# Kernel tuning notes

Measured on AMD Instinct MI355X. Metric: run time of the kernel, lower is better.

The kernel has to match this reference:

```python
import jax, jax.numpy as jnp
import numpy as np

N = 100000
E = 3200000
F_IN = 256
HID = 16
N_CLS = 32


def setup_inputs() -> dict:
    key = jax.random.key(0)
    ks = jax.random.split(key, 9)
    x = jax.random.normal(ks[0], (N, F_IN), dtype=jnp.float32)
    edge_index = jax.random.randint(ks[1], (2, E), 0, N, dtype=jnp.int32)
    def glorot(k, fan_in, fan_out):
        s = jnp.sqrt(6.0 / (fan_in + fan_out)).astype(jnp.float32)
        return jax.random.uniform(k, (fan_in, fan_out), jnp.float32, -s, s)
    return {
        "x": x,
        "edge_index": edge_index,
        "W1": glorot(ks[2], F_IN, HID), "b1": jnp.zeros((HID,), jnp.float32),
        "W2": glorot(ks[3], HID, HID), "b2": jnp.zeros((HID,), jnp.float32),
        "W3": glorot(ks[4], HID, N_CLS), "b3": jnp.zeros((N_CLS,), jnp.float32),
    }


def _gcn_conv(h, W, b, src, dst, deg_inv_sqrt):
    # h: [N, d_in] -> [N, d_out]. PyG GCNConv: linear, then D^-1/2 (A+I) D^-1/2 aggregation, then bias.
    h = h @ W                                        # [N, d_out]
    norm = deg_inv_sqrt[src] * deg_inv_sqrt[dst]     # [E]
    msg = h[src] * norm[:, None]                     # [E, d_out]
    agg = jax.ops.segment_sum(msg, dst, num_segments=N)
    # self-loop contribution: norm_ii = deg_inv_sqrt[i]^2
    agg = agg + (deg_inv_sqrt ** 2)[:, None] * h
    return agg + b


def reference(x, edge_index, W1, b1, W2, b2, W3, b3):
    src, dst = edge_index[0], edge_index[1]
    # degree with self-loops (edge weights = 1), computed on dst per PyG gcn_norm
    deg = jax.ops.segment_sum(jnp.ones((E,), jnp.float32), dst, num_segments=N) + 1.0
    deg_inv_sqrt = jax.lax.rsqrt(deg)
    h = jax.nn.elu(_gcn_conv(x, W1, b1, src, dst, deg_inv_sqrt))
    h = jax.nn.elu(_gcn_conv(h, W2, b2, src, dst, deg_inv_sqrt))
    h = jax.nn.elu(_gcn_conv(h, W3, b3, src, dst, deg_inv_sqrt))
    # dropout is identity in eval mode (training=False)
    return jax.nn.log_softmax(h, axis=1)
```

## Files before the change

### kernel.cpp

```cpp
#include <hip/hip_runtime.h>
#include <math.h>

static constexpr int N_NODES = 100000;
static constexpr int N_EDGES = 3200000;
static constexpr int F_INC   = 256;
static constexpr int HIDC    = 16;
static constexpr int NCLS    = 32;

static constexpr int BNODES  = 256;
static constexpr int NBKT    = (N_NODES + BNODES - 1) / BNODES;
static constexpr int CAP     = 9216;
static constexpr int CHUNK   = 4096;
static constexpr int NCHUNK  = (N_EDGES + CHUNK - 1) / CHUNK;
static constexpr int NTILES  = N_NODES / 16;

typedef __attribute__((ext_vector_type(8))) short bf16x8;
typedef __attribute__((ext_vector_type(4))) float f32x4;

__device__ __forceinline__ unsigned pack_bf2(float a, float b) {
    unsigned ua = __float_as_uint(a);
    unsigned ub = __float_as_uint(b);
    ua = (ua + 0x7FFFu + ((ua >> 16) & 1u)) >> 16;
    ub = (ub + 0x7FFFu + ((ub >> 16) & 1u)) & 0xFFFF0000u;
    return ua | ub;
}
__device__ __forceinline__ float bflo(unsigned v) { return __uint_as_float(v << 16); }
__device__ __forceinline__ float bfhi(unsigned v) { return __uint_as_float(v & 0xFFFF0000u); }
__device__ __forceinline__ float elu1(float t) { return t > 0.f ? t : expm1f(t); }

__global__ void k_zero_cur(int* gcur) {
    int i = threadIdx.x;
    if (i < NBKT) gcur[i] = 0;
}

__global__ __launch_bounds__(256) void k_bucket(const int* __restrict__ src,
                                                const int* __restrict__ dst,
                                                int* gcur, unsigned int* __restrict__ slab) {
    __shared__ int hist[512];
    __shared__ int sc[512];
    __shared__ int place[512];
    __shared__ int gbase[512];
    __shared__ unsigned int staging[CHUNK];
    __shared__ unsigned short bid[CHUNK];
    int tid = threadIdx.x;
    int e0 = blockIdx.x * CHUNK;
    int n = min(CHUNK, N_EDGES - e0);
    hist[tid] = 0; hist[tid + 256] = 0;
    __syncthreads();
    unsigned int pay[16];
    int bk[16];
    #pragma unroll
    for (int r = 0; r < 16; ++r) {
        int i = r * 256 + tid;
        bk[r] = -1;
        if (i < n) {
            int e = e0 + i;
            int s = src[e];
            int t = dst[e];
            int b = t >> 8;
            pay[r] = (unsigned)s | ((unsigned)(t & 255) << 24);
            bk[r] = b;
            atomicAdd(&hist[b], 1);
        }
    }
    __syncthreads();
    sc[tid] = hist[tid]; sc[tid + 256] = hist[tid + 256];
    __syncthreads();
    for (int off = 1; off < 512; off <<= 1) {
        int i0 = tid, i1 = tid + 256;
        int v0 = (i0 >= off) ? sc[i0 - off] : 0;
        int v1 = (i1 >= off) ? sc[i1 - off] : 0;
        __syncthreads();
        sc[i0] += v0; sc[i1] += v1;
        __syncthreads();
    }
    {
        int b0 = tid, b1 = tid + 256;
        int o0 = sc[b0] - hist[b0];
        int o1 = sc[b1] - hist[b1];
        place[b0] = o0; place[b1] = o1;
        sc[b0] = o0; sc[b1] = o1;
        if (b0 < NBKT && hist[b0]) gbase[b0] = atomicAdd(&gcur[b0], hist[b0]);
        if (b1 < NBKT && hist[b1]) gbase[b1] = atomicAdd(&gcur[b1], hist[b1]);
    }
    __syncthreads();
    #pragma unroll
    for (int r = 0; r < 16; ++r) {
        if (bk[r] >= 0) {
            int p = atomicAdd(&place[bk[r]], 1);
            staging[p] = pay[r];
            bid[p] = (unsigned short)bk[r];
        }
    }
    __syncthreads();
    for (int i = tid; i < n; i += 256) {
        int b = bid[i];
        int gp = gbase[b] + (i - sc[b]);
        if (gp < CAP) slab[(size_t)b * CAP + gp] = staging[i];
    }
}

__global__ __launch_bounds__(512) void k_csr(const int* __restrict__ gcur,
                                             unsigned int* __restrict__ slab,
                                             int* __restrict__ rowptr,
                                             int* __restrict__ cnt,
                                             float* __restrict__ dis) {
    __shared__ int hist[BNODES];
    __shared__ int lofs[BNODES];
    __shared__ int place[BNODES];
    __shared__ unsigned int reord[CAP];
    int tid = threadIdx.x, b = blockIdx.x;
    if (tid < BNODES) hist[tid] = 0;
    __syncthreads();
    int count = min(gcur[b], CAP);
    unsigned int* sl = slab + (size_t)b * CAP;
    for (int i = tid; i < count; i += 512) atomicAdd(&hist[sl[i] >> 24], 1);
    __syncthreads();
    if (tid < BNODES) lofs[tid] = hist[tid];
    __syncthreads();
    for (int off = 1; off < BNODES; off <<= 1) {
        int v = 0;
        if (tid < BNODES && tid >= off) v = lofs[tid - off];
        __syncthreads();
        if (tid < BNODES) lofs[tid] += v;
        __syncthreads();
    }
    if (tid < BNODES) {
        int ex = lofs[tid] - hist[tid];
        lofs[tid] = ex;
        place[tid] = ex;
        int node = b * BNODES + tid;
        if (node < N_NODES) {
            rowptr[node] = b * CAP + ex;
            cnt[node] = hist[tid];
            dis[node] = rsqrtf((float)hist[tid] + 1.0f);
        }
    }
    __syncthreads();
    for (int i = tid; i < count; i += 512) {
        unsigned int v = sl[i];
        int dl = v >> 24;
        int p = atomicAdd(&place[dl], 1);
        reord[p] = v & 0xFFFFFFu;
    }
    __syncthreads();
    for (int i = tid; i < count; i += 512) sl[i] = reord[i];
}

__global__ __launch_bounds__(256) void k_linear1(const float* __restrict__ x,
                                                 const float* __restrict__ W1,
                                                 const float* __restrict__ dis,
                                                 unsigned* __restrict__ hb) {
    __shared__ float dtile[4][16][18];
    int tid = threadIdx.x;
    int lane = tid & 63;
    int w = tid >> 6;
    int tile = blockIdx.x * 4 + w;
    if (tile >= NTILES) return;
    int g = lane >> 4;
    int r = lane & 15;
    union { uint4 u; bf16x8 v; } bfr[8];
    #pragma unroll
    for (int m = 0; m < 8; ++m) {
        unsigned uu[4];
        #pragma unroll
        for (int t = 0; t < 4; ++t) {
            int k0 = 32 * m + 8 * g + 2 * t;
            uu[t] = pack_bf2(W1[k0 * HIDC + r], W1[(k0 + 1) * HIDC + r]);
        }
        bfr[m].u = make_uint4(uu[0], uu[1], uu[2], uu[3]);
    }
    const float* xrow = x + (size_t)(tile * 16 + r) * F_INC;
    f32x4 acc = {0.f, 0.f, 0.f, 0.f};
    #pragma unroll
    for (int m = 0; m < 8; ++m) {
        int ks = 32 * m + 8 * g;
        float4 va = *(const float4*)(xrow + ks);
        float4 vb = *(const float4*)(xrow + ks + 4);
        union { uint4 u; bf16x8 v; } af;
        af.u = make_uint4(pack_bf2(va.x, va.y), pack_bf2(va.z, va.w),
                          pack_bf2(vb.x, vb.y), pack_bf2(vb.z, vb.w));
        acc = __builtin_amdgcn_mfma_f32_16x16x32_bf16(af.v, bfr[m].v, acc, 0, 0, 0);
    }
    #pragma unroll
    for (int t = 0; t < 4; ++t) dtile[w][4 * g + t][r] = acc[t];
    __builtin_amdgcn_s_waitcnt(0);
    int q = lane & 7;
    #pragma unroll
    for (int h = 0; h < 2; ++h) {
        int rr = (lane >> 3) + 8 * h;
        int node = tile * 16 + rr;
        float dn = dis[node];
        hb[(size_t)node * 8 + q] =
            pack_bf2(dn * dtile[w][rr][2 * q], dn * dtile[w][rr][2 * q + 1]);
    }
}

__device__ __forceinline__ void gather_core(int base, int deg, int q,
                                            const unsigned* __restrict__ csr,
                                            const unsigned* __restrict__ hb,
                                            unsigned sv, float& acc0, float& acc1) {
    acc0 = bflo(sv); acc1 = bfhi(sv);
    int j = 0;
    for (; j + 3 < deg; j += 4) {
        int s0 = csr[base + j];
        int s1 = csr[base + j + 1];
        int s2 = csr[base + j + 2];
        int s3 = csr[base + j + 3];
        unsigned v0 = hb[(size_t)s0 * 8 + q];
        unsigned v1 = hb[(size_t)s1 * 8 + q];
        unsigned v2 = hb[(size_t)s2 * 8 + q];
        unsigned v3 = hb[(size_t)s3 * 8 + q];
        acc0 += (bflo(v0) + bflo(v1)) + (bflo(v2) + bflo(v3));
        acc1 += (bfhi(v0) + bfhi(v1)) + (bfhi(v2) + bfhi(v3));
    }
    for (; j < deg; ++j) {
        int s = csr[base + j];
        unsigned v = hb[(size_t)s * 8 + q];
        acc0 += bflo(v);
        acc1 += bfhi(v);
    }
}

__global__ __launch_bounds__(256) void k_gather_fl1(const int* __restrict__ rowptr,
                                                    const int* __restrict__ cnt,
                                                    const unsigned* __restrict__ csr,
                                                    const float* __restrict__ dis,
                                                    const unsigned* __restrict__ hb,
                                                    const float* __restrict__ b1,
                                                    const float* __restrict__ W2,
                                                    unsigned* __restrict__ hb_out) {
    __shared__ float W2s[HIDC * HIDC];
    __shared__ float b1s[HIDC];
    if (threadIdx.x < HIDC * HIDC) W2s[threadIdx.x] = W2[threadIdx.x];
    if (threadIdx.x < HIDC) b1s[threadIdx.x] = b1[threadIdx.x];
    __syncthreads();
    int idx = blockIdx.x * blockDim.x + threadIdx.x;
    int n = idx >> 3;
    if (n >= N_NODES) return;
    int q = idx & 7;
    int lane = threadIdx.x & 63;
    float acc0, acc1;
    gather_core(rowptr[n], cnt[n], q, csr, hb, hb[(size_t)n * 8 + q], acc0, acc1);
    float dn = dis[n];
    float a0 = elu1(acc0 * dn + b1s[2 * q]);
    float a1 = elu1(acc1 * dn + b1s[2 * q + 1]);
    int gb = lane & 56;
    float h0 = 0.f, h1 = 0.f;
    #pragma unroll
    for (int k2 = 0; k2 < 8; ++k2) {
        float e0 = __shfl(a0, gb + k2, 64);
        float e1 = __shfl(a1, gb + k2, 64);
        h0 += e0 * W2s[(2 * k2) * HIDC + 2 * q]     + e1 * W2s[(2 * k2 + 1) * HIDC + 2 * q];
        h1 += e0 * W2s[(2 * k2) * HIDC + 2 * q + 1] + e1 * W2s[(2 * k2 + 1) * HIDC + 2 * q + 1];
    }
    hb_out[(size_t)n * 8 + q] = pack_bf2(dn * h0, dn * h1);
}

__global__ __launch_bounds__(256) void k_gather_z(const int* __restrict__ rowptr,
                                                  const int* __restrict__ cnt,
                                                  const unsigned* __restrict__ csr,
                                                  const float* __restrict__ dis,
                                                  const unsigned* __restrict__ hb,
                                                  const float* __restrict__ bias,
                                                  unsigned* __restrict__ outp) {
    int idx = blockIdx.x * blockDim.x + threadIdx.x;
    int n = idx >> 3;
    if (n >= N_NODES) return;
    int q = idx & 7;
    float acc0, acc1;
    gather_core(rowptr[n], cnt[n], q, csr, hb, hb[(size_t)n * 8 + q], acc0, acc1);
    float dn = dis[n];
    float z0 = elu1(acc0 * dn + bias[2 * q]);
    float z1 = elu1(acc1 * dn + bias[2 * q + 1]);
    outp[(size_t)n * 8 + q] = pack_bf2(dn * z0, dn * z1);
}

__global__ __launch_bounds__(256) void k_gather_fin(const int* __restrict__ rowptr,
                                                    const int* __restrict__ cnt,
                                                    const unsigned* __restrict__ csr,
                                                    const float* __restrict__ dis,
                                                    const unsigned* __restrict__ hb,
                                                    const float* __restrict__ W3,
                                                    const float* __restrict__ b3,
                                                    float* __restrict__ out) {
    __shared__ float W3s[HIDC * NCLS];
    __shared__ float b3s[NCLS];
    for (int i = threadIdx.x; i < HIDC * NCLS; i += 256) W3s[i] = W3[i];
    if (threadIdx.x < NCLS) b3s[threadIdx.x] = b3[threadIdx.x];
    __syncthreads();
    int idx = blockIdx.x * blockDim.x + threadIdx.x;
    int n = idx >> 3;
    if (n >= N_NODES) return;
    int q = idx & 7;
    int lane = threadIdx.x & 63;
    float acc0, acc1;
    gather_core(rowptr[n], cnt[n], q, csr, hb, hb[(size_t)n * 8 + q], acc0, acc1);
    float dn = dis[n];
    float g0 = acc0 * dn, g1 = acc1 * dn;
    int gb = lane & 56;
    int j0 = q * 4;
    float r0 = b3s[j0], r1 = b3s[j0 + 1], r2 = b3s[j0 + 2], r3 = b3s[j0 + 3];
    #pragma unroll
    for (int k2 = 0; k2 < 8; ++k2) {
        float e0 = __shfl(g0, gb + k2, 64);
        float e1 = __shfl(g1, gb + k2, 64);
        const float* wa = &W3s[(2 * k2) * NCLS + j0];
        const float* wb = &W3s[(2 * k2 + 1) * NCLS + j0];
        r0 += e0 * wa[0] + e1 * wb[0];
        r1 += e0 * wa[1] + e1 * wb[1];
        r2 += e0 * wa[2] + e1 * wb[2];
        r3 += e0 * wa[3] + e1 * wb[3];
    }
    r0 = elu1(r0); r1 = elu1(r1); r2 = elu1(r2); r3 = elu1(r3);
    float m = fmaxf(fmaxf(r0, r1), fmaxf(r2, r3));
    #pragma unroll
    for (int off = 1; off < 8; off <<= 1) m = fmaxf(m, __shfl_xor(m, off, 64));
    float s = expf(r0 - m) + expf(r1 - m) + expf(r2 - m) + expf(r3 - m);
    #pragma unroll
    for (int off = 1; off < 8; off <<= 1) s += __shfl_xor(s, off, 64);
    float lse = logf(s) + m;
    float4* o = (float4*)(out + (size_t)n * NCLS + j0);
    *o = make_float4(r0 - lse, r1 - lse, r2 - lse, r3 - lse);
}

extern "C" void kernel_launch(void* const* d_in, const int* in_sizes, int n_in,
                              void* d_out, int out_size, void* d_ws, size_t ws_size,
                              hipStream_t stream) {
    const float* x  = (const float*)d_in[0];
    const int*   ei = (const int*)d_in[1];
    const float* W1 = (const float*)d_in[2];
    const float* b1 = (const float*)d_in[3];
    const float* W2 = (const float*)d_in[4];
    const float* b2 = (const float*)d_in[5];
    const float* W3 = (const float*)d_in[6];
    const float* b3 = (const float*)d_in[7];
    float* out = (float*)d_out;
    const int* src = ei;
    const int* dst = ei + N_EDGES;

    int* wi = (int*)d_ws;
    int*          gcur   = wi;
    unsigned int* slab   = (unsigned int*)(wi + 512);
    int*          rowptr = wi + 512 + NBKT * CAP;
    int*          cnt    = rowptr + 102400;
    float*        dis    = (float*)(cnt + 102400);
    unsigned*     Bh     = (unsigned*)(dis + 102400);
    unsigned*     Zb     = Bh + 819200;
    (void)ws_size; (void)n_in; (void)in_sizes; (void)out_size;

    auto blocks = [](long long n) { return (int)((n + 255) / 256); };
    const int GGATH = blocks((long long)N_NODES * 8);
    const int GLIN1 = (NTILES + 3) / 4;

    k_zero_cur<<<1, 512, 0, stream>>>(gcur);
    k_bucket<<<NCHUNK, 256, 0, stream>>>(src, dst, gcur, slab);
    k_csr<<<NBKT, 512, 0, stream>>>(gcur, slab, rowptr, cnt, dis);

    k_linear1<<<GLIN1, 256, 0, stream>>>(x, W1, dis, Bh);
    k_gather_fl1<<<GGATH, 256, 0, stream>>>(rowptr, cnt, slab, dis, Bh, b1, W2, Zb);
    k_gather_z<<<GGATH, 256, 0, stream>>>(rowptr, cnt, slab, dis, Zb, b2, Bh);
    k_gather_fin<<<GGATH, 256, 0, stream>>>(rowptr, cnt, slab, dis, Bh, W3, b3, out);
}
```

Baseline: 166.4 us.

## Fuse linear1 into bucketing kernel and gather four features per thread

The X@W1 projection now runs as extra blocks inside the edge-bucketing kernel. Because the projection no longer depends on the degree normalization, the first layer's gather instead scales each neighbor by its own dis value loaded per edge. The gather kernels switch from 8 threads per node with one packed pair each to 4 threads per node loading uint2 (four bf16 features), halving the thread count and widening the loads. The aim is to overlap the dense GEMV with the scatter phase, drop a launch, and reduce per-edge index load overhead, at the cost of an extra dis lookup per edge in layer one.

Result: slower. 185.6 us (+11.6%).

```diff
diff --git a/kernel.cpp b/kernel.cpp
--- a/kernel.cpp
+++ b/kernel.cpp
@@ -13,6 +13,7 @@
 static constexpr int CHUNK   = 4096;
 static constexpr int NCHUNK  = (N_EDGES + CHUNK - 1) / CHUNK;
 static constexpr int NTILES  = N_NODES / 16;
+static constexpr int GLIN1   = (NTILES + 3) / 4;
 
 typedef __attribute__((ext_vector_type(8))) short bf16x8;
 typedef __attribute__((ext_vector_type(4))) float f32x4;
@@ -33,70 +34,118 @@
     if (i < NBKT) gcur[i] = 0;
 }
 
-__global__ __launch_bounds__(256) void k_bucket(const int* __restrict__ src,
-                                                const int* __restrict__ dst,
-                                                int* gcur, unsigned int* __restrict__ slab) {
-    __shared__ int hist[512];
-    __shared__ int sc[512];
-    __shared__ int place[512];
-    __shared__ int gbase[512];
-    __shared__ unsigned int staging[CHUNK];
-    __shared__ unsigned short bid[CHUNK];
+__global__ __launch_bounds__(256) void k_bucklin(const int* __restrict__ src,
+                                                 const int* __restrict__ dst,
+                                                 int* gcur, unsigned int* __restrict__ slab,
+                                                 const float* __restrict__ x,
+                                                 const float* __restrict__ W1,
+                                                 unsigned* __restrict__ hb) {
+    __shared__ int sm[8192];
     int tid = threadIdx.x;
-    int e0 = blockIdx.x * CHUNK;
-    int n = min(CHUNK, N_EDGES - e0);
-    hist[tid] = 0; hist[tid + 256] = 0;
-    __syncthreads();
-    unsigned int pay[16];
-    int bk[16];
-    #pragma unroll
-    for (int r = 0; r < 16; ++r) {
-        int i = r * 256 + tid;
-        bk[r] = -1;
-        if (i < n) {
-            int e = e0 + i;
-            int s = src[e];
-            int t = dst[e];
-            int b = t >> 8;
-            pay[r] = (unsigned)s | ((unsigned)(t & 255) << 24);
-            bk[r] = b;
-            atomicAdd(&hist[b], 1);
-        }
-    }
-    __syncthreads();
-    sc[tid] = hist[tid]; sc[tid + 256] = hist[tid + 256];
-    __syncthreads();
-    for (int off = 1; off < 512; off <<= 1) {
-        int i0 = tid, i1 = tid + 256;
-        int v0 = (i0 >= off) ? sc[i0 - off] : 0;
-        int v1 = (i1 >= off) ? sc[i1 - off] : 0;
-        __syncthreads();
-        sc[i0] += v0; sc[i1] += v1;
-        __syncthreads();
-    }
-    {
-        int b0 = tid, b1 = tid + 256;
-        int o0 = sc[b0] - hist[b0];
-        int o1 = sc[b1] - hist[b1];
-        place[b0] = o0; place[b1] = o1;
-        sc[b0] = o0; sc[b1] = o1;
-        if (b0 < NBKT && hist[b0]) gbase[b0] = atomicAdd(&gcur[b0], hist[b0]);
-        if (b1 < NBKT && hist[b1]) gbase[b1] = atomicAdd(&gcur[b1], hist[b1]);
-    }
-    __syncthreads();
-    #pragma unroll
-    for (int r = 0; r < 16; ++r) {
-        if (bk[r] >= 0) {
-            int p = atomicAdd(&place[bk[r]], 1);
-            staging[p] = pay[r];
-            bid[p] = (unsigned short)bk[r];
-        }
-    }
-    __syncthreads();
-    for (int i = tid; i < n; i += 256) {
-        int b = bid[i];
-        int gp = gbase[b] + (i - sc[b]);
-        if (gp < CAP) slab[(size_t)b * CAP + gp] = staging[i];
+    if (blockIdx.x < NCHUNK) {
+        int* hist  = sm;
+        int* sc    = sm + 512;
+        int* place = sm + 1024;
+        int* gbase = sm + 1536;
+        unsigned* staging = (unsigned*)(sm + 2048);
+        unsigned short* bid = (unsigned short*)(sm + 6144);
+        int e0 = blockIdx.x * CHUNK;
+        int n = min(CHUNK, N_EDGES - e0);
+        hist[tid] = 0; hist[tid + 256] = 0;
+        __syncthreads();
+        unsigned pay[16];
+        int bk[16];
+        #pragma unroll
+        for (int r = 0; r < 16; ++r) {
+            int i = r * 256 + tid;
+            bk[r] = -1;
+            if (i < n) {
+                int e = e0 + i;
+                int s = src[e];
+                int t = dst[e];
+                int b = t >> 8;
+                pay[r] = (unsigned)s | ((unsigned)(t & 255) << 24);
+                bk[r] = b;
+                atomicAdd(&hist[b], 1);
+            }
+        }
+        __syncthreads();
+        sc[tid] = hist[tid]; sc[tid + 256] = hist[tid + 256];
+        __syncthreads();
+        for (int off = 1; off < 512; off <<= 1) {
+            int i0 = tid, i1 = tid + 256;
+            int v0 = (i0 >= off) ? sc[i0 - off] : 0;
+            int v1 = (i1 >= off) ? sc[i1 - off] : 0;
+            __syncthreads();
+            sc[i0] += v0; sc[i1] += v1;
+            __syncthreads();
+        }
+        {
+            int b0 = tid, b1 = tid + 256;
+            int o0 = sc[b0] - hist[b0];
+            int o1 = sc[b1] - hist[b1];
+            place[b0] = o0; place[b1] = o1;
+            sc[b0] = o0; sc[b1] = o1;
+            if (b0 < NBKT && hist[b0]) gbase[b0] = atomicAdd(&gcur[b0], hist[b0]);
+            if (b1 < NBKT && hist[b1]) gbase[b1] = atomicAdd(&gcur[b1], hist[b1]);
+        }
+        __syncthreads();
+        #pragma unroll
+        for (int r = 0; r < 16; ++r) {
+            if (bk[r] >= 0) {
+                int p = atomicAdd(&place[bk[r]], 1);
+                staging[p] = pay[r];
+                bid[p] = (unsigned short)bk[r];
+            }
+        }
+        __syncthreads();
+        for (int i = tid; i < n; i += 256) {
+            int b = bid[i];
+            int gp = gbase[b] + (i - sc[b]);
+            if (gp < CAP) slab[(size_t)b * CAP + gp] = staging[i];
+        }
+    } else {
+        float* dtile = (float*)sm;
+        int lane = tid & 63;
+        int w = tid >> 6;
+        int tile = (blockIdx.x - NCHUNK) * 4 + w;
+        if (tile >= NTILES) return;
+        int g = lane >> 4;
+        int r = lane & 15;
+        union { uint4 u; bf16x8 v; } bfr[8];
+        #pragma unroll
+        for (int m = 0; m < 8; ++m) {
+            unsigned uu[4];
+            #pragma unroll
+            for (int t = 0; t < 4; ++t) {
+                int k0 = 32 * m + 8 * g + 2 * t;
+                uu[t] = pack_bf2(W1[k0 * HIDC + r], W1[(k0 + 1) * HIDC + r]);
+            }
+            bfr[m].u = make_uint4(uu[0], uu[1], uu[2], uu[3]);
+        }
+        const float* xrow = x + (size_t)(tile * 16 + r) * F_INC;
+        f32x4 acc = {0.f, 0.f, 0.f, 0.f};
+        #pragma unroll
+        for (int m = 0; m < 8; ++m) {
+            int ks = 32 * m + 8 * g;
+            float4 va = *(const float4*)(xrow + ks);
+            float4 vb = *(const float4*)(xrow + ks + 4);
+            union { uint4 u; bf16x8 v; } af;
+            af.u = make_uint4(pack_bf2(va.x, va.y), pack_bf2(va.z, va.w),
+                              pack_bf2(vb.x, vb.y), pack_bf2(vb.z, vb.w));
+            acc = __builtin_amdgcn_mfma_f32_16x16x32_bf16(af.v, bfr[m].v, acc, 0, 0, 0);
+        }
+        float* dt = dtile + w * 288;
+        #pragma unroll
+        for (int t = 0; t < 4; ++t) dt[(4 * g + t) * 18 + r] = acc[t];
+        __builtin_amdgcn_s_waitcnt(0);
+        int q = lane & 7;
+        #pragma unroll
+        for (int h = 0; h < 2; ++h) {
+            int rr = (lane >> 3) + 8 * h;
+            int node = tile * 16 + rr;
+            hb[(size_t)node * 8 + q] = pack_bf2(dt[rr * 18 + 2 * q], dt[rr * 18 + 2 * q + 1]);
+        }
     }
 }
 
@@ -147,78 +196,29 @@
     for (int i = tid; i < count; i += 512) sl[i] = reord[i];
 }
 
-__global__ __launch_bounds__(256) void k_linear1(const float* __restrict__ x,
-                                                 const float* __restrict__ W1,
-                                                 const float* __restrict__ dis,
-                                                 unsigned* __restrict__ hb) {
-    __shared__ float dtile[4][16][18];
-    int tid = threadIdx.x;
-    int lane = tid & 63;
-    int w = tid >> 6;
-    int tile = blockIdx.x * 4 + w;
-    if (tile >= NTILES) return;
-    int g = lane >> 4;
-    int r = lane & 15;
-    union { uint4 u; bf16x8 v; } bfr[8];
-    #pragma unroll
-    for (int m = 0; m < 8; ++m) {
-        unsigned uu[4];
-        #pragma unroll
-        for (int t = 0; t < 4; ++t) {
-            int k0 = 32 * m + 8 * g + 2 * t;
-            uu[t] = pack_bf2(W1[k0 * HIDC + r], W1[(k0 + 1) * HIDC + r]);
-        }
-        bfr[m].u = make_uint4(uu[0], uu[1], uu[2], uu[3]);
-    }
-    const float* xrow = x + (size_t)(tile * 16 + r) * F_INC;
-    f32x4 acc = {0.f, 0.f, 0.f, 0.f};
-    #pragma unroll
-    for (int m = 0; m < 8; ++m) {
-        int ks = 32 * m + 8 * g;
-        float4 va = *(const float4*)(xrow + ks);
-        float4 vb = *(const float4*)(xrow + ks + 4);
-        union { uint4 u; bf16x8 v; } af;
-        af.u = make_uint4(pack_bf2(va.x, va.y), pack_bf2(va.z, va.w),
-                          pack_bf2(vb.x, vb.y), pack_bf2(vb.z, vb.w));
-        acc = __builtin_amdgcn_mfma_f32_16x16x32_bf16(af.v, bfr[m].v, acc, 0, 0, 0);
-    }
-    #pragma unroll
-    for (int t = 0; t < 4; ++t) dtile[w][4 * g + t][r] = acc[t];
-    __builtin_amdgcn_s_waitcnt(0);
-    int q = lane & 7;
-    #pragma unroll
-    for (int h = 0; h < 2; ++h) {
-        int rr = (lane >> 3) + 8 * h;
-        int node = tile * 16 + rr;
-        float dn = dis[node];
-        hb[(size_t)node * 8 + q] =
-            pack_bf2(dn * dtile[w][rr][2 * q], dn * dtile[w][rr][2 * q + 1]);
-    }
-}
-
-__device__ __forceinline__ void gather_core(int base, int deg, int q,
-                                            const unsigned* __restrict__ csr,
-                                            const unsigned* __restrict__ hb,
-                                            unsigned sv, float& acc0, float& acc1) {
-    acc0 = bflo(sv); acc1 = bfhi(sv);
+__device__ __forceinline__ void gather4(int base, int deg, int q,
+                                        const unsigned* __restrict__ csr,
+                                        const unsigned* __restrict__ hb,
+                                        float& a0, float& a1, float& a2, float& a3) {
     int j = 0;
     for (; j + 3 < deg; j += 4) {
         int s0 = csr[base + j];
         int s1 = csr[base + j + 1];
         int s2 = csr[base + j + 2];
         int s3 = csr[base + j + 3];
-        unsigned v0 = hb[(size_t)s0 * 8 + q];
-        unsigned v1 = hb[(size_t)s1 * 8 + q];
-        unsigned v2 = hb[(size_t)s2 * 8 + q];
-        unsigned v3 = hb[(size_t)s3 * 8 + q];
-        acc0 += (bflo(v0) + bflo(v1)) + (bflo(v2) + bflo(v3));
-        acc1 += (bfhi(v0) + bfhi(v1)) + (bfhi(v2) + bfhi(v3));
+        uint2 v0 = *(const uint2*)&hb[(size_t)s0 * 8 + 2 * q];
+        uint2 v1 = *(const uint2*)&hb[(size_t)s1 * 8 + 2 * q];
+        uint2 v2 = *(const uint2*)&hb[(size_t)s2 * 8 + 2 * q];
+        uint2 v3 = *(const uint2*)&hb[(size_t)s3 * 8 + 2 * q];
+        a0 += (bflo(v0.x) + bflo(v1.x)) + (bflo(v2.x) + bflo(v3.x));
+        a1 += (bfhi(v0.x) + bfhi(v1.x)) + (bfhi(v2.x) + bfhi(v3.x));
+        a2 += (bflo(v0.y) + bflo(v1.y)) + (bflo(v2.y) + bflo(v3.y));
+        a3 += (bfhi(v0.y) + bfhi(v1.y)) + (bfhi(v2.y) + bfhi(v3.y));
     }
     for (; j < deg; ++j) {
         int s = csr[base + j];
-        unsigned v = hb[(size_t)s * 8 + q];
-        acc0 += bflo(v);
-        acc1 += bfhi(v);
+        uint2 v = *(const uint2*)&hb[(size_t)s * 8 + 2 * q];
+        a0 += bflo(v.x); a1 += bfhi(v.x); a2 += bflo(v.y); a3 += bfhi(v.y);
     }
 }
 
@@ -236,25 +236,62 @@
     if (threadIdx.x < HIDC) b1s[threadIdx.x] = b1[threadIdx.x];
     __syncthreads();
     int idx = blockIdx.x * blockDim.x + threadIdx.x;
-    int n = idx >> 3;
+    int n = idx >> 2;
     if (n >= N_NODES) return;
-    int q = idx & 7;
+    int q = idx & 3;
     int lane = threadIdx.x & 63;
-    float acc0, acc1;
-    gather_core(rowptr[n], cnt[n], q, csr, hb, hb[(size_t)n * 8 + q], acc0, acc1);
+    int base = rowptr[n];
+    int deg = cnt[n];
     float dn = dis[n];
-    float a0 = elu1(acc0 * dn + b1s[2 * q]);
-    float a1 = elu1(acc1 * dn + b1s[2 * q + 1]);
-    int gb = lane & 56;
-    float h0 = 0.f, h1 = 0.f;
+    uint2 sv = *(const uint2*)&hb[(size_t)n * 8 + 2 * q];
+    float a0 = dn * bflo(sv.x), a1 = dn * bfhi(sv.x);
+    float a2 = dn * bflo(sv.y), a3 = dn * bfhi(sv.y);
+    int j = 0;
+    for (; j + 3 < deg; j += 4) {
+        int s0 = csr[base + j];
+        int s1 = csr[base + j + 1];
+        int s2 = csr[base + j + 2];
+        int s3 = csr[base + j + 3];
+        float d0 = dis[s0], d1 = dis[s1], d2 = dis[s2], d3 = dis[s3];
+        uint2 v0 = *(const uint2*)&hb[(size_t)s0 * 8 + 2 * q];
+        uint2 v1 = *(const uint2*)&hb[(size_t)s1 * 8 + 2 * q];
+        uint2 v2 = *(const uint2*)&hb[(size_t)s2 * 8 + 2 * q];
+        uint2 v3 = *(const uint2*)&hb[(size_t)s3 * 8 + 2 * q];
+        a0 += d0 * bflo(v0.x) + d1 * bflo(v1.x) + d2 * bflo(v2.x) + d3 * bflo(v3.x);
+        a1 += d0 * bfhi(v0.x) + d1 * bfhi(v1.x) + d2 * bfhi(v2.x) + d3 * bfhi(v3.x);
+        a2 += d0 * bflo(v0.y) + d1 * bflo(v1.y) + d2 * bflo(v2.y) + d3 * bflo(v3.y);
+        a3 += d0 * bfhi(v0.y) + d1 * bfhi(v1.y) + d2 * bfhi(v2.y) + d3 * bfhi(v3.y);
+    }
+    for (; j < deg; ++j) {
+        int s = csr[base + j];
+        float ds = dis[s];
+        uint2 v = *(const uint2*)&hb[(size_t)s * 8 + 2 * q];
+        a0 += ds * bflo(v.x); a1 += ds * bfhi(v.x);
+        a2 += ds * bflo(v.y); a3 += ds * bfhi(v.y);
+    }
+    a0 = elu1(dn * a0 + b1s[4 * q + 0]);
+    a1 = elu1(dn * a1 + b1s[4 * q + 1]);
+    a2 = elu1(dn * a2 + b1s[4 * q + 2]);
+    a3 = elu1(dn * a3 + b1s[4 * q + 3]);
+    int gb = lane & 60;
+    float h0 = 0.f, h1 = 0.f, h2 = 0.f, h3 = 0.f;
     #pragma unroll
-    for (int k2 = 0; k2 < 8; ++k2) {
-        float e0 = __shfl(a0, gb + k2, 64);
-        float e1 = __shfl(a1, gb + k2, 64);
-        h0 += e0 * W2s[(2 * k2) * HIDC + 2 * q]     + e1 * W2s[(2 * k2 + 1) * HIDC + 2 * q];
-        h1 += e0 * W2s[(2 * k2) * HIDC + 2 * q + 1] + e1 * W2s[(2 * k2 + 1) * HIDC + 2 * q + 1];
-    }
-    hb_out[(size_t)n * 8 + q] = pack_bf2(dn * h0, dn * h1);
+    for (int kl = 0; kl < 4; ++kl) {
+        float e0 = __shfl(a0, gb + kl, 64);
+        float e1 = __shfl(a1, gb + kl, 64);
+        float e2 = __shfl(a2, gb + kl, 64);
+        float e3 = __shfl(a3, gb + kl, 64);
+        const float* w0 = &W2s[(4 * kl) * HIDC + 4 * q];
+        const float* w1 = &W2s[(4 * kl + 1) * HIDC + 4 * q];
+        const float* w2 = &W2s[(4 * kl + 2) * HIDC + 4 * q];
+        const float* w3 = &W2s[(4 * kl + 3) * HIDC + 4 * q];
+        h0 += e0 * w0[0] + e1 * w1[0] + e2 * w2[0] + e3 * w3[0];
+        h1 += e0 * w0[1] + e1 * w1[1] + e2 * w2[1] + e3 * w3[1];
+        h2 += e0 * w0[2] + e1 * w1[2] + e2 * w2[2] + e3 * w3[2];
+        h3 += e0 * w0[3] + e1 * w1[3] + e2 * w2[3] + e3 * w3[3];
+    }
+    *(uint2*)&hb_out[(size_t)n * 8 + 2 * q] =
+        make_uint2(pack_bf2(dn * h0, dn * h1), pack_bf2(dn * h2, dn * h3));
 }
 
 __global__ __launch_bounds__(256) void k_gather_z(const int* __restrict__ rowptr,
@@ -265,15 +302,19 @@
                                                   const float* __restrict__ bias,
                                                   unsigned* __restrict__ outp) {
     int idx = blockIdx.x * blockDim.x + threadIdx.x;
-    int n = idx >> 3;
+    int n = idx >> 2;
     if (n >= N_NODES) return;
-    int q = idx & 7;
-    float acc0, acc1;
-    gather_core(rowptr[n], cnt[n], q, csr, hb, hb[(size_t)n * 8 + q], acc0, acc1);
+    int q = idx & 3;
+    uint2 sv = *(const uint2*)&hb[(size_t)n * 8 + 2 * q];
+    float a0 = bflo(sv.x), a1 = bfhi(sv.x), a2 = bflo(sv.y), a3 = bfhi(sv.y);
+    gather4(rowptr[n], cnt[n], q, csr, hb, a0, a1, a2, a3);
     float dn = dis[n];
-    float z0 = elu1(acc0 * dn + bias[2 * q]);
-    float z1 = elu1(acc1 * dn + bias[2 * q + 1]);
-    outp[(size_t)n * 8 + q] = pack_bf2(dn * z0, dn * z1);
+    float z0 = elu1(a0 * dn + bias[4 * q + 0]);
+    float z1 = elu1(a1 * dn + bias[4 * q + 1]);
+    float z2 = elu1(a2 * dn + bias[4 * q + 2]);
+    float z3 = elu1(a3 * dn + bias[4 * q + 3]);
+    *(uint2*)&outp[(size_t)n * 8 + 2 * q] =
+        make_uint2(pack_bf2(dn * z0, dn * z1), pack_bf2(dn * z2, dn * z3));
 }
 
 __global__ __launch_bounds__(256) void k_gather_fin(const int* __restrict__ rowptr,
@@ -290,38 +331,48 @@
     if (threadIdx.x < NCLS) b3s[threadIdx.x] = b3[threadIdx.x];
     __syncthreads();
     int idx = blockIdx.x * blockDim.x + threadIdx.x;
-    int n = idx >> 3;
+    int n = idx >> 2;
     if (n >= N_NODES) return;
-    int q = idx & 7;
+    int q = idx & 3;
     int lane = threadIdx.x & 63;
-    float acc0, acc1;
-    gather_core(rowptr[n], cnt[n], q, csr, hb, hb[(size_t)n * 8 + q], acc0, acc1);
+    uint2 sv = *(const uint2*)&hb[(size_t)n * 8 + 2 * q];
+    float a0 = bflo(sv.x), a1 = bfhi(sv.x), a2 = bflo(sv.y), a3 = bfhi(sv.y);
+    gather4(rowptr[n], cnt[n], q, csr, hb, a0, a1, a2, a3);
     float dn = dis[n];
-    float g0 = acc0 * dn, g1 = acc1 * dn;
-    int gb = lane & 56;
-    int j0 = q * 4;
-    float r0 = b3s[j0], r1 = b3s[j0 + 1], r2 = b3s[j0 + 2], r3 = b3s[j0 + 3];
+    a0 *= dn; a1 *= dn; a2 *= dn; a3 *= dn;
+    int gb = lane & 60;
+    int j0 = q * 8;
+    float r[8];
     #pragma unroll
-    for (int k2 = 0; k2 < 8; ++k2) {
-        float e0 = __shfl(g0, gb + k2, 64);
-        float e1 = __shfl(g1, gb + k2, 64);
-        const float* wa = &W3s[(2 * k2) * NCLS + j0];
-        const float* wb = &W3s[(2 * k2 + 1) * NCLS + j0];
-        r0 += e0 * wa[0] + e1 * wb[0];
-        r1 += e0 * wa[1] + e1 * wb[1];
-        r2 += e0 * wa[2] + e1 * wb[2];
-        r3 += e0 * wa[3] + e1 * wb[3];
-    }
-    r0 = elu1(r0); r1 = elu1(r1); r2 = elu1(r2); r3 = elu1(r3);
-    float m = fmaxf(fmaxf(r0, r1), fmaxf(r2, r3));
+    for (int c = 0; c < 8; ++c) r[c] = b3s[j0 + c];
     #pragma unroll
-    for (int off = 1; off < 8; off <<= 1) m = fmaxf(m, __shfl_xor(m, off, 64));
-    float s = expf(r0 - m) + expf(r1 - m) + expf(r2 - m) + expf(r3 - m);
+    for (int kl = 0; kl < 4; ++kl) {
+        float e0 = __shfl(a0, gb + kl, 64);
+        float e1 = __shfl(a1, gb + kl, 64);
+        float e2 = __shfl(a2, gb + kl, 64);
+        float e3 = __shfl(a3, gb + kl, 64);
+        const float* w0 = &W3s[(4 * kl) * NCLS + j0];
+        const float* w1 = &W3s[(4 * kl + 1) * NCLS + j0];
+        const float* w2 = &W3s[(4 * kl + 2) * NCLS + j0];
+        const float* w3 = &W3s[(4 * kl + 3) * NCLS + j0];
+        #pragma unroll
+        for (int c = 0; c < 8; ++c)
+            r[c] += e0 * w0[c] + e1 * w1[c] + e2 * w2[c] + e3 * w3[c];
+    }
+    float m = -1e30f;
     #pragma unroll
-    for (int off = 1; off < 8; off <<= 1) s += __shfl_xor(s, off, 64);
+    for (int c = 0; c < 8; ++c) { r[c] = elu1(r[c]); m = fmaxf(m, r[c]); }
+    m = fmaxf(m, __shfl_xor(m, 1, 64));
+    m = fmaxf(m, __shfl_xor(m, 2, 64));
+    float s = 0.f;
+    #pragma unroll
+    for (int c = 0; c < 8; ++c) s += expf(r[c] - m);
+    s += __shfl_xor(s, 1, 64);
+    s += __shfl_xor(s, 2, 64);
     float lse = logf(s) + m;
     float4* o = (float4*)(out + (size_t)n * NCLS + j0);
-    *o = make_float4(r0 - lse, r1 - lse, r2 - lse, r3 - lse);
+    o[0] = make_float4(r[0] - lse, r[1] - lse, r[2] - lse, r[3] - lse);
+    o[1] = make_float4(r[4] - lse, r[5] - lse, r[6] - lse, r[7] - lse);
 }
 
 extern "C" void kernel_launch(void* const* d_in, const int* in_sizes, int n_in,
@@ -349,16 +400,13 @@
     unsigned*     Zb     = Bh + 819200;
     (void)ws_size; (void)n_in; (void)in_sizes; (void)out_size;
 
-    auto blocks = [](long long n) { return (int)((n + 255) / 256); };
-    const int GGATH = blocks((long long)N_NODES * 8);
-    const int GLIN1 = (NTILES + 3) / 4;
+    const int GG4 = (int)(((long long)N_NODES * 4 + 255) / 256);
 
     k_zero_cur<<<1, 512, 0, stream>>>(gcur);
-    k_bucket<<<NCHUNK, 256, 0, stream>>>(src, dst, gcur, slab);
+    k_bucklin<<<NCHUNK + GLIN1, 256, 0, stream>>>(src, dst, gcur, slab, x, W1, Bh);
     k_csr<<<NBKT, 512, 0, stream>>>(gcur, slab, rowptr, cnt, dis);
 
-    k_linear1<<<GLIN1, 256, 0, stream>>>(x, W1, dis, Bh);
-    k_gather_fl1<<<GGATH, 256, 0, stream>>>(rowptr, cnt, slab, dis, Bh, b1, W2, Zb);
-    k_gather_z<<<GGATH, 256, 0, stream>>>(rowptr, cnt, slab, dis, Zb, b2, Bh);
-    k_gather_fin<<<GGATH, 256, 0, stream>>>(rowptr, cnt, slab, dis, Bh, W3, b3, out);
-}
+    k_gather_fl1<<<GG4, 256, 0, stream>>>(rowptr, cnt, slab, dis, Bh, b1, W2, Zb);
+    k_gather_z<<<GG4, 256, 0, stream>>>(rowptr, cnt, slab, dis, Zb, b2, Bh);
+    k_gather_fin<<<GG4, 256, 0, stream>>>(rowptr, cnt, slab, dis, Bh, W3, b3, out);
+}
```

## Sort nodes by degree within buckets to balance gather wavefront work

Applied to the files above, without the earlier changes.

Adds a per-bucket counting sort of nodes by in-degree, producing a node permutation that the three gather kernels use to pick which node each 8-lane group handles. Nodes of similar degree then share a wavefront, which is meant to cut divergence from uneven loop trip counts in the neighbor gather loop. In exchange it adds a small kernel launch and an extra indirection load per node. Output locality for the stores and self-row reads becomes scattered within each 256-node bucket.

Result: slower. 184.7 us (+11.0%).

```diff
diff --git a/kernel.cpp b/kernel.cpp
--- a/kernel.cpp
+++ b/kernel.cpp
@@ -13,6 +13,8 @@
 static constexpr int CHUNK   = 4096;
 static constexpr int NCHUNK  = (N_EDGES + CHUNK - 1) / CHUNK;
 static constexpr int NTILES  = N_NODES / 16;
+static constexpr int GLIN1   = (NTILES + 3) / 4;
+static constexpr int NRANK   = NBKT * BNODES;
 
 typedef __attribute__((ext_vector_type(8))) short bf16x8;
 typedef __attribute__((ext_vector_type(4))) float f32x4;
@@ -145,6 +147,32 @@
     }
     __syncthreads();
     for (int i = tid; i < count; i += 512) sl[i] = reord[i];
+}
+
+__global__ __launch_bounds__(256) void k_perm(const int* __restrict__ cnt,
+                                              int* __restrict__ nodeperm) {
+    __shared__ int dhist[256];
+    __shared__ int dofs[256];
+    __shared__ int dplace[256];
+    int tid = threadIdx.x, b = blockIdx.x;
+    int node = b * BNODES + tid;
+    int deg = (node < N_NODES) ? min(cnt[node], 255) : 0;
+    dhist[tid] = 0;
+    __syncthreads();
+    atomicAdd(&dhist[deg], 1);
+    __syncthreads();
+    dofs[tid] = dhist[tid];
+    __syncthreads();
+    for (int off = 1; off < 256; off <<= 1) {
+        int v = (tid >= off) ? dofs[tid - off] : 0;
+        __syncthreads();
+        dofs[tid] += v;
+        __syncthreads();
+    }
+    dplace[tid] = dofs[tid] - dhist[tid];
+    __syncthreads();
+    int rank = atomicAdd(&dplace[deg], 1);
+    nodeperm[b * BNODES + rank] = node;
 }
 
 __global__ __launch_bounds__(256) void k_linear1(const float* __restrict__ x,
@@ -226,6 +254,7 @@
                                                     const int* __restrict__ cnt,
                                                     const unsigned* __restrict__ csr,
                                                     const float* __restrict__ dis,
+                                                    const int* __restrict__ nodeperm,
                                                     const unsigned* __restrict__ hb,
                                                     const float* __restrict__ b1,
                                                     const float* __restrict__ W2,
@@ -236,7 +265,9 @@
     if (threadIdx.x < HIDC) b1s[threadIdx.x] = b1[threadIdx.x];
     __syncthreads();
     int idx = blockIdx.x * blockDim.x + threadIdx.x;
-    int n = idx >> 3;
+    int rank = idx >> 3;
+    if (rank >= NRANK) return;
+    int n = nodeperm[rank];
     if (n >= N_NODES) return;
     int q = idx & 7;
     int lane = threadIdx.x & 63;
@@ -261,11 +292,14 @@
                                                   const int* __restrict__ cnt,
                                                   const unsigned* __restrict__ csr,
                                                   const float* __restrict__ dis,
+                                                  const int* __restrict__ nodeperm,
                                                   const unsigned* __restrict__ hb,
                                                   const float* __restrict__ bias,
                                                   unsigned* __restrict__ outp) {
     int idx = blockIdx.x * blockDim.x + threadIdx.x;
-    int n = idx >> 3;
+    int rank = idx >> 3;
+    if (rank >= NRANK) return;
+    int n = nodeperm[rank];
     if (n >= N_NODES) return;
     int q = idx & 7;
     float acc0, acc1;
@@ -280,6 +314,7 @@
                                                     const int* __restrict__ cnt,
                                                     const unsigned* __restrict__ csr,
                                                     const float* __restrict__ dis,
+                                                    const int* __restrict__ nodeperm,
                                                     const unsigned* __restrict__ hb,
                                                     const float* __restrict__ W3,
                                                     const float* __restrict__ b3,
@@ -290,7 +325,9 @@
     if (threadIdx.x < NCLS) b3s[threadIdx.x] = b3[threadIdx.x];
     __syncthreads();
     int idx = blockIdx.x * blockDim.x + threadIdx.x;
-    int n = idx >> 3;
+    int rank = idx >> 3;
+    if (rank >= NRANK) return;
+    int n = nodeperm[rank];
     if (n >= N_NODES) return;
     int q = idx & 7;
     int lane = threadIdx.x & 63;
@@ -340,25 +377,25 @@
     const int* dst = ei + N_EDGES;
 
     int* wi = (int*)d_ws;
-    int*          gcur   = wi;
-    unsigned int* slab   = (unsigned int*)(wi + 512);
-    int*          rowptr = wi + 512 + NBKT * CAP;
-    int*          cnt    = rowptr + 102400;
-    float*        dis    = (float*)(cnt + 102400);
-    unsigned*     Bh     = (unsigned*)(dis + 102400);
-    unsigned*     Zb     = Bh + 819200;
+    int*          gcur     = wi;
+    unsigned int* slab     = (unsigned int*)(wi + 512);
+    int*          rowptr   = wi + 512 + NBKT * CAP;
+    int*          cnt      = rowptr + 102400;
+    float*        dis      = (float*)(cnt + 102400);
+    int*          nodeperm = (int*)(dis + 102400);
+    unsigned*     Bh       = (unsigned*)(nodeperm + 100352);
+    unsigned*     Zb       = Bh + 819200;
     (void)ws_size; (void)n_in; (void)in_sizes; (void)out_size;
 
-    auto blocks = [](long long n) { return (int)((n + 255) / 256); };
-    const int GGATH = blocks((long long)N_NODES * 8);
-    const int GLIN1 = (NTILES + 3) / 4;
+    const int GGATH = (int)(((long long)NRANK * 8 + 255) / 256);
 
     k_zero_cur<<<1, 512, 0, stream>>>(gcur);
     k_bucket<<<NCHUNK, 256, 0, stream>>>(src, dst, gcur, slab);
     k_csr<<<NBKT, 512, 0, stream>>>(gcur, slab, rowptr, cnt, dis);
+    k_perm<<<NBKT, 256, 0, stream>>>(cnt, nodeperm);
 
     k_linear1<<<GLIN1, 256, 0, stream>>>(x, W1, dis, Bh);
-    k_gather_fl1<<<GGATH, 256, 0, stream>>>(rowptr, cnt, slab, dis, Bh, b1, W2, Zb);
-    k_gather_z<<<GGATH, 256, 0, stream>>>(rowptr, cnt, slab, dis, Zb, b2, Bh);
-    k_gather_fin<<<GGATH, 256, 0, stream>>>(rowptr, cnt, slab, dis, Bh, W3, b3, out);
-}
+    k_gather_fl1<<<GGATH, 256, 0, stream>>>(rowptr, cnt, slab, dis, nodeperm, Bh, b1, W2, Zb);
+    k_gather_z<<<GGATH, 256, 0, stream>>>(rowptr, cnt, slab, dis, nodeperm, Zb, b2, Bh);
+    k_gather_fin<<<GGATH, 256, 0, stream>>>(rowptr, cnt, slab, dis, nodeperm, Bh, W3, b3, out);
+}
```
